# Kernel tuning notes

Measured on AMD Instinct MI355X. Metric: run time of the kernel, lower is better.

Reference implementation:

```python
import jax, jax.numpy as jnp
import numpy as np

B, TQ, TV, H = 8, 2048, 2048, 1024
LN_EPS = 1e-5


def setup_inputs() -> dict:
    key = jax.random.key(0)
    k1, k2, k3, k4 = jax.random.split(key, 4)
    query = jax.random.normal(k1, (B, TQ, H), dtype=jnp.float32)
    value = jax.random.normal(k2, (B, TV, H), dtype=jnp.float32)
    # nn.Linear(2H -> H): weight [H, 2H], bias [H]
    bound = 1.0 / np.sqrt(2 * H)
    W = jax.random.uniform(k3, (H, 2 * H), minval=-bound, maxval=bound, dtype=jnp.float32)
    b = jax.random.uniform(k4, (H,), minval=-bound, maxval=bound, dtype=jnp.float32)
    gamma = jnp.ones((H,), dtype=jnp.float32)
    beta = jnp.zeros((H,), dtype=jnp.float32)
    return {"query": query, "value": value, "W": W, "b": b, "gamma": gamma, "beta": beta}


def reference(query, value, W, b, gamma, beta):
    # scores: [B, Tq, Tv]
    score = jnp.einsum("bqh,bvh->bqv", query, value)
    attn = jax.nn.softmax(score, axis=-1)
    context = jnp.einsum("bqv,bvh->bqh", attn, value)  # [B, Tq, H]
    combined = jnp.concatenate((context, query), axis=2)  # [B, Tq, 2H]
    proj = jnp.einsum("bqk,hk->bqh", combined, W) + b  # [B, Tq, H]
    mean = jnp.mean(proj, axis=-1, keepdims=True)
    var = jnp.mean(jnp.square(proj - mean), axis=-1, keepdims=True)
    out = (proj - mean) * jax.lax.rsqrt(var + LN_EPS) * gamma + beta
    return out
```

## Files before the change

kernel.cpp:

```cpp
#include <hip/hip_runtime.h>

typedef unsigned short u16;
typedef _Float16 f16;
typedef __attribute__((ext_vector_type(8))) _Float16 f16x8;
typedef __attribute__((ext_vector_type(4))) float f32x4;

#define B_  8
#define TQ_ 2048
#define TV_ 2048
#define H_  1024

__device__ __forceinline__ u16 f2h(float x) {
    union { f16 h; u16 u; } c; c.h = (f16)x; return c.u;
}

__device__ __forceinline__ void gload_lds16(const u16* g, u16* l) {
    typedef __attribute__((address_space(1))) const unsigned short GAS;
    typedef __attribute__((address_space(3))) unsigned short LAS;
    __builtin_amdgcn_global_load_lds((GAS*)g, (LAS*)l, 16, 0, 0);
}

__global__ __launch_bounds__(256) void k_cvt(const float4* __restrict__ x,
                                             ushort4* __restrict__ o) {
    long long i = (long long)blockIdx.x * 256 + threadIdx.x;
    float4 v = x[i];
    ushort4 h;
    h.x = f2h(v.x); h.y = f2h(v.y); h.z = f2h(v.z); h.w = f2h(v.w);
    o[i] = h;
}

__global__ __launch_bounds__(256) void k_cvt_q(const float4* __restrict__ q4,
                                               u16* __restrict__ CQ) {
    long long i = (long long)blockIdx.x * 256 + threadIdx.x;
    float4 x = q4[i];
    ushort4 h;
    h.x = f2h(x.x); h.y = f2h(x.y); h.z = f2h(x.z); h.w = f2h(x.w);
    long long row = i >> 8;
    int col = (int)(i & 255) * 4;
    *(ushort4*)(CQ + row * 2048 + 1024 + col) = h;
}

__global__ __launch_bounds__(256) void k_cvt_vt(const float* __restrict__ v,
                                                u16* __restrict__ Vh,
                                                u16* __restrict__ VT) {
    __shared__ u16 s[64][65];
    const int t = threadIdx.x;
    const int c0 = blockIdx.x * 64;
    const int r0 = blockIdx.y * 64;
    const long long zb = (long long)blockIdx.z * (2048LL * 1024LL);
    const float* ib = v + zb;
#pragma unroll
    for (int it = 0; it < 4; ++it) {
        int rl = it * 16 + (t >> 4);
        int cl = (t & 15) * 4;
        float4 x = *(const float4*)(ib + (long long)(r0 + rl) * 1024 + c0 + cl);
        ushort4 h;
        h.x = f2h(x.x); h.y = f2h(x.y); h.z = f2h(x.z); h.w = f2h(x.w);
        *(ushort4*)(Vh + zb + (long long)(r0 + rl) * 1024 + c0 + cl) = h;
        s[rl][cl + 0] = h.x; s[rl][cl + 1] = h.y; s[rl][cl + 2] = h.z; s[rl][cl + 3] = h.w;
    }
    __syncthreads();
#pragma unroll
    for (int it = 0; it < 4; ++it) {
        int cl = it * 16 + (t >> 4);
        int rl = (t & 15) * 4;
        ushort4 o;
        o.x = s[rl + 0][cl]; o.y = s[rl + 1][cl]; o.z = s[rl + 2][cl]; o.w = s[rl + 3][cl];
        *(ushort4*)(VT + zb + (long long)(c0 + cl) * 2048 + r0 + rl) = o;
    }
}

#define SBAR() __builtin_amdgcn_sched_barrier(0)

template<int NH, int OM, int LDA, int LDB, int KK>
__global__ __launch_bounds__(512, 2) void k_gemm8(const u16* __restrict__ Ap,
                                                  const u16* __restrict__ Bp,
                                                  long long sA, long long sB,
                                                  int mnTiles, int gn,
                                                  void* __restrict__ Cv, long long sC,
                                                  int ldc, const float* __restrict__ bias) {
    constexpr int BUFU = 16384 + NH * 8192;
    constexpr int NT = KK / 64;
    __shared__ __align__(16) u16 lds[2 * BUFU];

    const int nper = gridDim.x >> 3;
    const int g = (blockIdx.x & 7) * nper + (blockIdx.x >> 3);
    const int z = g / mnTiles;
    const int rem = g - z * mnTiles;
    const int bm = (rem / gn) * 256;
    const int bn = (rem % gn) * (NH * 128);

    const int tid = threadIdx.x;
    const int lane = tid & 63, wid = tid >> 6;
    const int wm = wid >> 2, wn = wid & 3;
    const int l16 = lane & 15, kg = lane >> 4;

    f32x4 acc[8][NH * 2];
    f32x4 zv = {0.f, 0.f, 0.f, 0.f};
#pragma unroll
    for (int i = 0; i < 8; ++i)
#pragma unroll
        for (int j = 0; j < NH * 2; ++j) acc[i][j] = zv;

    const u16* Ab = Ap + (long long)z * sA;
    const u16* Bb = Bp + (long long)z * sB;

    const int jst = (tid & 7) ^ ((tid >> 3) & 7);
    const int rst = tid >> 3;

    auto stageA = [&](int k0, int h, int obase) {
#pragma unroll
        for (int c = 0; c < 2; ++c) {
            int r = h * 128 + c * 64 + rst;
            gload_lds16(Ab + (long long)(bm + r) * LDA + k0 + jst * 8,
                        &lds[obase + h * 8192 + c * 4096 + tid * 8]);
        }
    };
    auto stageB = [&](int k0, int h, int rbase) {
#pragma unroll
        for (int c = 0; c < 2; ++c) {
            int r = h * 128 + c * 64 + rst;
            gload_lds16(Bb + (long long)(bn + r) * LDB + k0 + jst * 8,
                        &lds[rbase + h * 8192 + c * 4096 + tid * 8]);
        }
    };
    auto rdA = [&](int base, int mh, f16x8* dst) {
#pragma unroll
        for (int i = 0; i < 4; ++i) {
            int r = wm * 128 + mh * 64 + i * 16 + l16;
#pragma unroll
            for (int ks = 0; ks < 2; ++ks) {
                int js = (ks * 4 + kg) ^ (r & 7);
                dst[i * 2 + ks] = *(const f16x8*)&lds[base + r * 64 + js * 8];
            }
        }
    };
    auto rdB = [&](int base, int nh, f16x8* dst) {
#pragma unroll
        for (int jn = 0; jn < 2; ++jn) {
            int r = wn * (NH * 32) + nh * 32 + jn * 16 + l16;
#pragma unroll
            for (int ks = 0; ks < 2; ++ks) {
                int js = (ks * 4 + kg) ^ (r & 7);
                dst[jn * 2 + ks] = *(const f16x8*)&lds[base + r * 64 + js * 8];
            }
        }
    };

    stageA(0, 0, 0);
    stageA(0, 1, 0);
#pragma unroll
    for (int h = 0; h < NH; ++h) stageB(0, h, 16384);
    if (NT > 1) {
#pragma unroll
        for (int h = 0; h < NH; ++h) stageB(64, h, BUFU + 16384);
        if constexpr (NH == 2) asm volatile("s_waitcnt vmcnt(4)" ::: "memory");
        else                   asm volatile("s_waitcnt vmcnt(2)" ::: "memory");
    } else {
        asm volatile("s_waitcnt vmcnt(0)" ::: "memory");
    }
    __builtin_amdgcn_s_barrier();
    SBAR();

    f16x8 a0[8], a1[8], b0[4], b1[4];
#pragma unroll 1
    for (int t = 0; t < NT; ++t) {
        const int cur = t & 1;
        const int AB = cur * BUFU;
        const int BB = AB + 16384;
        const int OA = (cur ^ 1) * BUFU;
        const bool sa = (t + 1) < NT;
        const bool sb = (t + 2) < NT;
        if constexpr (NH == 2) {
            rdA(AB, 0, a0);
            rdB(BB, 0, b0);
            rdB(BB, 1, b1);
            if (sa) stageA((t + 1) * 64, 0, OA);
            SBAR();
            __builtin_amdgcn_s_setprio(1);
#pragma unroll
            for (int i = 0; i < 4; ++i)
#pragma unroll
                for (int jn = 0; jn < 2; ++jn)
#pragma unroll
                    for (int ks = 0; ks < 2; ++ks)
                        acc[i][jn] = __builtin_amdgcn_mfma_f32_16x16x32_f16(a0[i * 2 + ks], b0[jn * 2 + ks], acc[i][jn], 0, 0, 0);
            __builtin_amdgcn_s_setprio(0);
            __builtin_amdgcn_s_barrier();
            SBAR();
            rdA(AB, 1, a1);
            if (sa) stageA((t + 1) * 64, 1, OA);
            SBAR();
            __builtin_amdgcn_s_setprio(1);
#pragma unroll
            for (int i = 0; i < 4; ++i)
#pragma unroll
                for (int jn = 0; jn < 2; ++jn)
#pragma unroll
                    for (int ks = 0; ks < 2; ++ks)
                        acc[i][2 + jn] = __builtin_amdgcn_mfma_f32_16x16x32_f16(a0[i * 2 + ks], b1[jn * 2 + ks], acc[i][2 + jn], 0, 0, 0);
            __builtin_amdgcn_s_setprio(0);
            __builtin_amdgcn_s_barrier();
            SBAR();
            if (sb) stageB((t + 2) * 64, 0, BB);
            SBAR();
            __builtin_amdgcn_s_setprio(1);
#pragma unroll
            for (int i = 0; i < 4; ++i)
#pragma unroll
                for (int jn = 0; jn < 2; ++jn)
#pragma unroll
                    for (int ks = 0; ks < 2; ++ks)
                        acc[4 + i][2 + jn] = __builtin_amdgcn_mfma_f32_16x16x32_f16(a1[i * 2 + ks], b1[jn * 2 + ks], acc[4 + i][2 + jn], 0, 0, 0);
            __builtin_amdgcn_s_setprio(0);
            __builtin_amdgcn_s_barrier();
            SBAR();
            if (sb) stageB((t + 2) * 64, 1, BB);
            SBAR();
            __builtin_amdgcn_s_setprio(1);
#pragma unroll
            for (int i = 0; i < 4; ++i)
#pragma unroll
                for (int jn = 0; jn < 2; ++jn)
#pragma unroll
                    for (int ks = 0; ks < 2; ++ks)
                        acc[4 + i][jn] = __builtin_amdgcn_mfma_f32_16x16x32_f16(a1[i * 2 + ks], b0[jn * 2 + ks], acc[4 + i][jn], 0, 0, 0);
            __builtin_amdgcn_s_setprio(0);
            if (sb)      asm volatile("s_waitcnt vmcnt(4)" ::: "memory");
            else if (sa) asm volatile("s_waitcnt vmcnt(0)" ::: "memory");
            __builtin_amdgcn_s_barrier();
            SBAR();
        } else {
            rdA(AB, 0, a0);
            rdB(BB, 0, b0);
            rdA(AB, 1, a1);
            if (sa) {
                stageA((t + 1) * 64, 0, OA);
                stageA((t + 1) * 64, 1, OA);
            }
            SBAR();
            __builtin_amdgcn_s_setprio(1);
#pragma unroll
            for (int i = 0; i < 4; ++i)
#pragma unroll
                for (int jn = 0; jn < 2; ++jn)
#pragma unroll
                    for (int ks = 0; ks < 2; ++ks)
                        acc[i][jn] = __builtin_amdgcn_mfma_f32_16x16x32_f16(a0[i * 2 + ks], b0[jn * 2 + ks], acc[i][jn], 0, 0, 0);
            __builtin_amdgcn_s_setprio(0);
            __builtin_amdgcn_s_barrier();
            SBAR();
            if (sb) stageB((t + 2) * 64, 0, BB);
            SBAR();
            __builtin_amdgcn_s_setprio(1);
#pragma unroll
            for (int i = 0; i < 4; ++i)
#pragma unroll
                for (int jn = 0; jn < 2; ++jn)
#pragma unroll
                    for (int ks = 0; ks < 2; ++ks)
                        acc[4 + i][jn] = __builtin_amdgcn_mfma_f32_16x16x32_f16(a1[i * 2 + ks], b0[jn * 2 + ks], acc[4 + i][jn], 0, 0, 0);
            __builtin_amdgcn_s_setprio(0);
            if (sb)      asm volatile("s_waitcnt vmcnt(2)" ::: "memory");
            else if (sa) asm volatile("s_waitcnt vmcnt(0)" ::: "memory");
            __builtin_amdgcn_s_barrier();
            SBAR();
        }
    }

    const int colBase = bn + wn * (NH * 32);
    const int rowBase = bm + wm * 128;
#pragma unroll
    for (int mi = 0; mi < 8; ++mi) {
#pragma unroll
        for (int nj = 0; nj < NH * 2; ++nj) {
            int col = colBase + nj * 16 + l16;
            float badd = bias ? bias[col] : 0.f;
#pragma unroll
            for (int r = 0; r < 4; ++r) {
                long long row = rowBase + mi * 16 + kg * 4 + r;
                long long idx = (long long)z * sC + row * (long long)ldc + col;
                float vv = acc[mi][nj][r] + badd;
                if constexpr (OM == 1) ((u16*)Cv)[idx] = f2h(vv);
                else ((float*)Cv)[idx] = vv;
            }
        }
    }
}

__global__ __launch_bounds__(256) void k_softmax(float* __restrict__ S) {
    float* row = S + (long long)blockIdx.x * TV_;
    u16* prow = (u16*)row;
    int t = threadIdx.x;
    float4 a = *(const float4*)(row + t * 4);
    float4 c = *(const float4*)(row + 1024 + t * 4);
    float m = fmaxf(fmaxf(fmaxf(a.x, a.y), fmaxf(a.z, a.w)),
                    fmaxf(fmaxf(c.x, c.y), fmaxf(c.z, c.w)));
#pragma unroll
    for (int o = 32; o; o >>= 1) m = fmaxf(m, __shfl_xor(m, o));
    __shared__ float rm[4], rs[4];
    if ((t & 63) == 0) rm[t >> 6] = m;
    __syncthreads();
    m = fmaxf(fmaxf(rm[0], rm[1]), fmaxf(rm[2], rm[3]));
    float e0 = __expf(a.x - m), e1 = __expf(a.y - m), e2 = __expf(a.z - m), e3 = __expf(a.w - m);
    float e4 = __expf(c.x - m), e5 = __expf(c.y - m), e6 = __expf(c.z - m), e7 = __expf(c.w - m);
    float s = ((e0 + e1) + (e2 + e3)) + ((e4 + e5) + (e6 + e7));
#pragma unroll
    for (int o = 32; o; o >>= 1) s += __shfl_xor(s, o);
    if ((t & 63) == 0) rs[t >> 6] = s;
    __syncthreads();
    s = rs[0] + rs[1] + rs[2] + rs[3];
    float inv = 1.f / s;
    ushort4 o0, o1;
    o0.x = f2h(e0 * inv); o0.y = f2h(e1 * inv); o0.z = f2h(e2 * inv); o0.w = f2h(e3 * inv);
    o1.x = f2h(e4 * inv); o1.y = f2h(e5 * inv); o1.z = f2h(e6 * inv); o1.w = f2h(e7 * inv);
    __syncthreads();
    *(ushort4*)(prow + t * 4) = o0;
    *(ushort4*)(prow + 1024 + t * 4) = o1;
}

__global__ __launch_bounds__(256) void k_layernorm(float* __restrict__ O,
                                                   const float* __restrict__ g,
                                                   const float* __restrict__ b) {
    float* row = O + (long long)blockIdx.x * H_;
    int t = threadIdx.x;
    float4 x = *(const float4*)(row + t * 4);
    float s1 = x.x + x.y + x.z + x.w;
    float s2 = x.x * x.x + x.y * x.y + x.z * x.z + x.w * x.w;
#pragma unroll
    for (int o = 32; o; o >>= 1) { s1 += __shfl_xor(s1, o); s2 += __shfl_xor(s2, o); }
    __shared__ float r1[4], r2[4];
    if ((t & 63) == 0) { r1[t >> 6] = s1; r2[t >> 6] = s2; }
    __syncthreads();
    s1 = r1[0] + r1[1] + r1[2] + r1[3];
    s2 = r2[0] + r2[1] + r2[2] + r2[3];
    float mean = s1 * (1.f / H_);
    float var = s2 * (1.f / H_) - mean * mean;
    float rstd = rsqrtf(fmaxf(var, 0.f) + 1e-5f);
    float4 gv = *(const float4*)(g + t * 4);
    float4 bv = *(const float4*)(b + t * 4);
    float4 o;
    o.x = (x.x - mean) * rstd * gv.x + bv.x;
    o.y = (x.y - mean) * rstd * gv.y + bv.y;
    o.z = (x.z - mean) * rstd * gv.z + bv.z;
    o.w = (x.w - mean) * rstd * gv.w + bv.w;
    *(float4*)(row + t * 4) = o;
}

extern "C" void kernel_launch(void* const* d_in, const int* in_sizes, int n_in,
                              void* d_out, int out_size, void* d_ws, size_t ws_size,
                              hipStream_t stream) {
    const float* q     = (const float*)d_in[0];
    const float* v     = (const float*)d_in[1];
    const float* W     = (const float*)d_in[2];
    const float* bias  = (const float*)d_in[3];
    const float* gamma = (const float*)d_in[4];
    const float* beta  = (const float*)d_in[5];
    float* out = (float*)d_out;
    char* ws = (char*)d_ws;

    const long long nQV = (long long)B_ * TQ_ * H_;
    const long long nW  = (long long)H_ * 2 * H_;
    const long long nCQ = (long long)B_ * TQ_ * 2048;

    u16* Vh = (u16*)ws;
    u16* VT = Vh + nQV;
    u16* Wh = VT + nQV;
    u16* CQ = Wh + nW;
    float* S = (float*)(CQ + nCQ);
    size_t fixedBytes = (size_t)((char*)S - ws);
    const size_t perZ = (size_t)TQ_ * TV_ * 4;

    int Zc = 1;
    for (int cand = 4; cand >= 1; cand >>= 1) {
        if (fixedBytes + (size_t)cand * perZ <= ws_size) { Zc = cand; break; }
    }

    k_cvt_q<<<dim3(nQV / 4 / 256), dim3(256), 0, stream>>>((const float4*)q, CQ);
    k_cvt  <<<dim3(nW / 4 / 256),  dim3(256), 0, stream>>>((const float4*)W, (ushort4*)Wh);
    k_cvt_vt<<<dim3(H_ / 64, TV_ / 64, B_), dim3(256), 0, stream>>>(v, Vh, VT);

    for (int c0 = 0; c0 < B_; c0 += Zc) {
        k_gemm8<2, 0, 2048, 1024, 1024><<<dim3(Zc * 64), dim3(512), 0, stream>>>(
            CQ + (long long)c0 * TQ_ * 2048 + 1024, Vh + (long long)c0 * TV_ * H_,
            (long long)TQ_ * 2048, (long long)TV_ * H_,
            64, 8, S, (long long)TQ_ * TV_, TV_, nullptr);
        k_softmax<<<dim3(Zc * TQ_), dim3(256), 0, stream>>>(S);
        k_gemm8<1, 1, 4096, 2048, 2048><<<dim3(Zc * 64), dim3(512), 0, stream>>>(
            (const u16*)S, VT + (long long)c0 * H_ * TV_,
            (long long)TQ_ * 4096, (long long)H_ * TV_,
            64, 8, CQ + (long long)c0 * TQ_ * 2048, (long long)TQ_ * 2048, 2048, nullptr);
    }

    k_gemm8<2, 0, 2048, 2048, 2048><<<dim3(256), dim3(512), 0, stream>>>(
        CQ, Wh, 0, 0, 256, 4, out, 0, H_, bias);

    k_layernorm<<<dim3(B_ * TQ_), dim3(256), 0, stream>>>(out, gamma, beta);
}
```

Baseline: 317.2 us.

## Fold output projection into attention via precomputed V·Wc and Q·Wq

This uses the linearity of the projection: proj = attn·(V·Wcᵀ) + Q·Wqᵀ + b. V·Wcᵀ (stored transposed) and Q·Wqᵀ are computed up front in fp16, and the second attention GEMM writes fp32 output directly, adding bias and the Q·Wq term in its epilogue. This removes the separate V transpose kernel, the concatenated buffer and the final K=2048 projection GEMM. It also merges stage steps in the NH=2 main-loop schedule to cut barriers. The trade-off is an extra rounding of the intermediate products to fp16 and different total GEMM work per phase.

```diff
diff --git a/kernel.cpp b/kernel.cpp
--- a/kernel.cpp
+++ b/kernel.cpp
@@ -12,6 +12,9 @@
 
 __device__ __forceinline__ u16 f2h(float x) {
     union { f16 h; u16 u; } c; c.h = (f16)x; return c.u;
+}
+__device__ __forceinline__ float h2f(u16 u) {
+    union { u16 u; f16 h; } c; c.u = u; return (float)c.h;
 }
 
 __device__ __forceinline__ void gload_lds16(const u16* g, u16* l) {
@@ -29,47 +32,6 @@
     o[i] = h;
 }
 
-__global__ __launch_bounds__(256) void k_cvt_q(const float4* __restrict__ q4,
-                                               u16* __restrict__ CQ) {
-    long long i = (long long)blockIdx.x * 256 + threadIdx.x;
-    float4 x = q4[i];
-    ushort4 h;
-    h.x = f2h(x.x); h.y = f2h(x.y); h.z = f2h(x.z); h.w = f2h(x.w);
-    long long row = i >> 8;
-    int col = (int)(i & 255) * 4;
-    *(ushort4*)(CQ + row * 2048 + 1024 + col) = h;
-}
-
-__global__ __launch_bounds__(256) void k_cvt_vt(const float* __restrict__ v,
-                                                u16* __restrict__ Vh,
-                                                u16* __restrict__ VT) {
-    __shared__ u16 s[64][65];
-    const int t = threadIdx.x;
-    const int c0 = blockIdx.x * 64;
-    const int r0 = blockIdx.y * 64;
-    const long long zb = (long long)blockIdx.z * (2048LL * 1024LL);
-    const float* ib = v + zb;
-#pragma unroll
-    for (int it = 0; it < 4; ++it) {
-        int rl = it * 16 + (t >> 4);
-        int cl = (t & 15) * 4;
-        float4 x = *(const float4*)(ib + (long long)(r0 + rl) * 1024 + c0 + cl);
-        ushort4 h;
-        h.x = f2h(x.x); h.y = f2h(x.y); h.z = f2h(x.z); h.w = f2h(x.w);
-        *(ushort4*)(Vh + zb + (long long)(r0 + rl) * 1024 + c0 + cl) = h;
-        s[rl][cl + 0] = h.x; s[rl][cl + 1] = h.y; s[rl][cl + 2] = h.z; s[rl][cl + 3] = h.w;
-    }
-    __syncthreads();
-#pragma unroll
-    for (int it = 0; it < 4; ++it) {
-        int cl = it * 16 + (t >> 4);
-        int rl = (t & 15) * 4;
-        ushort4 o;
-        o.x = s[rl + 0][cl]; o.y = s[rl + 1][cl]; o.z = s[rl + 2][cl]; o.w = s[rl + 3][cl];
-        *(ushort4*)(VT + zb + (long long)(c0 + cl) * 2048 + r0 + rl) = o;
-    }
-}
-
 #define SBAR() __builtin_amdgcn_sched_barrier(0)
 
 template<int NH, int OM, int LDA, int LDB, int KK>
@@ -78,7 +40,8 @@
                                                   long long sA, long long sB,
                                                   int mnTiles, int gn,
                                                   void* __restrict__ Cv, long long sC,
-                                                  int ldc, const float* __restrict__ bias) {
+                                                  int ldc, const float* __restrict__ bias,
+                                                  const u16* __restrict__ qadd) {
     constexpr int BUFU = 16384 + NH * 8192;
     constexpr int NT = KK / 64;
     __shared__ __align__(16) u16 lds[2 * BUFU];
@@ -175,7 +138,10 @@
             rdA(AB, 0, a0);
             rdB(BB, 0, b0);
             rdB(BB, 1, b1);
-            if (sa) stageA((t + 1) * 64, 0, OA);
+            if (sa) {
+                stageA((t + 1) * 64, 0, OA);
+                stageA((t + 1) * 64, 1, OA);
+            }
             SBAR();
             __builtin_amdgcn_s_setprio(1);
 #pragma unroll
@@ -185,13 +151,6 @@
 #pragma unroll
                     for (int ks = 0; ks < 2; ++ks)
                         acc[i][jn] = __builtin_amdgcn_mfma_f32_16x16x32_f16(a0[i * 2 + ks], b0[jn * 2 + ks], acc[i][jn], 0, 0, 0);
-            __builtin_amdgcn_s_setprio(0);
-            __builtin_amdgcn_s_barrier();
-            SBAR();
-            rdA(AB, 1, a1);
-            if (sa) stageA((t + 1) * 64, 1, OA);
-            SBAR();
-            __builtin_amdgcn_s_setprio(1);
 #pragma unroll
             for (int i = 0; i < 4; ++i)
 #pragma unroll
@@ -202,7 +161,11 @@
             __builtin_amdgcn_s_setprio(0);
             __builtin_amdgcn_s_barrier();
             SBAR();
-            if (sb) stageB((t + 2) * 64, 0, BB);
+            rdA(AB, 1, a1);
+            if (sb) {
+                stageB((t + 2) * 64, 0, BB);
+                stageB((t + 2) * 64, 1, BB);
+            }
             SBAR();
             __builtin_amdgcn_s_setprio(1);
 #pragma unroll
@@ -212,12 +175,6 @@
 #pragma unroll
                     for (int ks = 0; ks < 2; ++ks)
                         acc[4 + i][2 + jn] = __builtin_amdgcn_mfma_f32_16x16x32_f16(a1[i * 2 + ks], b1[jn * 2 + ks], acc[4 + i][2 + jn], 0, 0, 0);
-            __builtin_amdgcn_s_setprio(0);
-            __builtin_amdgcn_s_barrier();
-            SBAR();
-            if (sb) stageB((t + 2) * 64, 1, BB);
-            SBAR();
-            __builtin_amdgcn_s_setprio(1);
 #pragma unroll
             for (int i = 0; i < 4; ++i)
 #pragma unroll
@@ -275,14 +232,19 @@
 #pragma unroll
         for (int nj = 0; nj < NH * 2; ++nj) {
             int col = colBase + nj * 16 + l16;
-            float badd = bias ? bias[col] : 0.f;
+            float badd = (OM != 1 && bias) ? bias[col] : 0.f;
 #pragma unroll
             for (int r = 0; r < 4; ++r) {
                 long long row = rowBase + mi * 16 + kg * 4 + r;
                 long long idx = (long long)z * sC + row * (long long)ldc + col;
                 float vv = acc[mi][nj][r] + badd;
-                if constexpr (OM == 1) ((u16*)Cv)[idx] = f2h(vv);
-                else ((float*)Cv)[idx] = vv;
+                if constexpr (OM == 1) {
+                    ((u16*)Cv)[idx] = f2h(vv);
+                } else if constexpr (OM == 2) {
+                    ((float*)Cv)[idx] = vv + h2f(qadd[idx]);
+                } else {
+                    ((float*)Cv)[idx] = vv;
+                }
             }
         }
     }
@@ -361,13 +323,13 @@
 
     const long long nQV = (long long)B_ * TQ_ * H_;
     const long long nW  = (long long)H_ * 2 * H_;
-    const long long nCQ = (long long)B_ * TQ_ * 2048;
-
-    u16* Vh = (u16*)ws;
-    u16* VT = Vh + nQV;
-    u16* Wh = VT + nQV;
-    u16* CQ = Wh + nW;
-    float* S = (float*)(CQ + nCQ);
+
+    u16* Qh  = (u16*)ws;
+    u16* Vh  = Qh + nQV;
+    u16* Wh  = Vh + nQV;
+    u16* VWT = Wh + nW;
+    u16* QW  = VWT + nQV;
+    float* S = (float*)(QW + nQV);
     size_t fixedBytes = (size_t)((char*)S - ws);
     const size_t perZ = (size_t)TQ_ * TV_ * 4;
 
@@ -376,24 +338,30 @@
         if (fixedBytes + (size_t)cand * perZ <= ws_size) { Zc = cand; break; }
     }
 
-    k_cvt_q<<<dim3(nQV / 4 / 256), dim3(256), 0, stream>>>((const float4*)q, CQ);
-    k_cvt  <<<dim3(nW / 4 / 256),  dim3(256), 0, stream>>>((const float4*)W, (ushort4*)Wh);
-    k_cvt_vt<<<dim3(H_ / 64, TV_ / 64, B_), dim3(256), 0, stream>>>(v, Vh, VT);
+    k_cvt<<<dim3(nQV / 4 / 256), dim3(256), 0, stream>>>((const float4*)q, (ushort4*)Qh);
+    k_cvt<<<dim3(nQV / 4 / 256), dim3(256), 0, stream>>>((const float4*)v, (ushort4*)Vh);
+    k_cvt<<<dim3(nW / 4 / 256),  dim3(256), 0, stream>>>((const float4*)W, (ushort4*)Wh);
+
+    k_gemm8<2, 1, 2048, 1024, 1024><<<dim3(256), dim3(512), 0, stream>>>(
+        Wh, Vh, 0, (long long)TV_ * H_,
+        32, 8, VWT, (long long)H_ * TV_, TV_, nullptr, nullptr);
+
+    k_gemm8<2, 1, 1024, 2048, 1024><<<dim3(256), dim3(512), 0, stream>>>(
+        Qh, Wh + H_, 0, 0,
+        256, 4, QW, 0, H_, nullptr, nullptr);
 
     for (int c0 = 0; c0 < B_; c0 += Zc) {
-        k_gemm8<2, 0, 2048, 1024, 1024><<<dim3(Zc * 64), dim3(512), 0, stream>>>(
-            CQ + (long long)c0 * TQ_ * 2048 + 1024, Vh + (long long)c0 * TV_ * H_,
-            (long long)TQ_ * 2048, (long long)TV_ * H_,
-            64, 8, S, (long long)TQ_ * TV_, TV_, nullptr);
+        k_gemm8<2, 0, 1024, 1024, 1024><<<dim3(Zc * 64), dim3(512), 0, stream>>>(
+            Qh + (long long)c0 * TQ_ * H_, Vh + (long long)c0 * TV_ * H_,
+            (long long)TQ_ * H_, (long long)TV_ * H_,
+            64, 8, S, (long long)TQ_ * TV_, TV_, nullptr, nullptr);
         k_softmax<<<dim3(Zc * TQ_), dim3(256), 0, stream>>>(S);
-        k_gemm8<1, 1, 4096, 2048, 2048><<<dim3(Zc * 64), dim3(512), 0, stream>>>(
-            (const u16*)S, VT + (long long)c0 * H_ * TV_,
+        k_gemm8<1, 2, 4096, 2048, 2048><<<dim3(Zc * 64), dim3(512), 0, stream>>>(
+            (const u16*)S, VWT + (long long)c0 * H_ * TV_,
             (long long)TQ_ * 4096, (long long)H_ * TV_,
-            64, 8, CQ + (long long)c0 * TQ_ * 2048, (long long)TQ_ * 2048, 2048, nullptr);
-    }
-
-    k_gemm8<2, 0, 2048, 2048, 2048><<<dim3(256), dim3(512), 0, stream>>>(
-        CQ, Wh, 0, 0, 256, 4, out, 0, H_, bias);
+            64, 8, out + (long long)c0 * TQ_ * H_, (long long)TQ_ * H_, H_,
+            bias, QW + (long long)c0 * TQ_ * H_);
+    }
 
     k_layernorm<<<dim3(B_ * TQ_), dim3(256), 0, stream>>>(out, gamma, beta);
 }
```

Result: no change. 323.4 us, median of 4 (+2.0%).
